# Kernel tuning notes

Hardware: AMD Instinct MI355X
Metric: run time of the kernel (lower is better)

## Reference

```python
import jax, jax.numpy as jnp
import numpy as np

B, T, C, H = 2, 2048, 1024, 16
D = C // H
HID = 4 * C
EPS = 1e-5


def _rmsnorm(x, w):
    return w * (x * jax.lax.rsqrt(jnp.mean(x * x, axis=-1, keepdims=True) + EPS))


def setup_inputs() -> dict:
    key = jax.random.key(0)
    ks = jax.random.split(key, 12)
    s = 0.02
    inp = {
        "x": jax.random.normal(ks[0], (B, T, C), jnp.float32),
        "mask": jnp.tril(jnp.ones((T, T), jnp.int32))[None, None],  # (1,1,T,T) causal
        "attn_norm_w": jnp.ones((C,), jnp.float32),
        "mlp_norm_w": jnp.ones((C,), jnp.float32),
        "q_w": jax.random.normal(ks[1], (C, C), jnp.float32) * s,
        "q_b": jnp.zeros((C,), jnp.float32),
        "k_w": jax.random.normal(ks[2], (C, C), jnp.float32) * s,
        "k_b": jnp.zeros((C,), jnp.float32),
        "v_w": jax.random.normal(ks[3], (C, C), jnp.float32) * s,
        "v_b": jnp.zeros((C,), jnp.float32),
        "o_w": jax.random.normal(ks[4], (C, C), jnp.float32) * s,
        "o_b": jnp.zeros((C,), jnp.float32),
        "w1": jax.random.normal(ks[5], (C, HID), jnp.float32) * s,
        "b1": jnp.zeros((HID,), jnp.float32),
        "w2": jax.random.normal(ks[6], (HID, C), jnp.float32) * s,
        "b2": jnp.zeros((C,), jnp.float32),
    }
    return inp


def reference(x, mask, attn_norm_w, mlp_norm_w, q_w, q_b, k_w, k_b, v_w, v_b,
              o_w, o_b, w1, b1, w2, b2):
    # Pre-norm path (use_post_norm=False)
    h = _rmsnorm(x, attn_norm_w)
    q = (h @ q_w + q_b).reshape(B, T, H, D).transpose(0, 2, 1, 3)  # (B,H,T,D)
    k = (h @ k_w + k_b).reshape(B, T, H, D).transpose(0, 2, 1, 3)
    v = (h @ v_w + v_b).reshape(B, T, H, D).transpose(0, 2, 1, 3)
    scores = jnp.einsum("bhqd,bhkd->bhqk", q, k) / jnp.sqrt(jnp.float32(D))
    scores = jnp.where(mask == 0, jnp.float32(-jnp.inf), scores)
    attn = jax.nn.softmax(scores, axis=-1)  # (B,H,T,T)
    ctx = jnp.einsum("bhqk,bhkd->bhqd", attn, v)
    attn_out = ctx.transpose(0, 2, 1, 3).reshape(B, T, C) @ o_w + o_b
    x = x + attn_out
    m = _rmsnorm(x, mlp_norm_w)
    mlp_out = jax.nn.gelu(m @ w1 + b1, approximate=False) @ w2 + b2
    x = x + mlp_out
    return (x, k, v)
```

## Files before the change

kernel.cpp:

```cpp
#include <hip/hip_runtime.h>
#include <hip/hip_bf16.h>


#define B_ 2
#define T_ 2048
#define C_ 1024
#define H_ 16
#define D_ 64
#define HID_ 4096
#define M_ 4096

typedef __bf16 bf16x8 __attribute__((ext_vector_type(8)));
typedef float f32x4 __attribute__((ext_vector_type(4)));
using bf16 = __hip_bfloat16;

#define WAIT_VM(N) asm volatile("s_waitcnt vmcnt(" #N ")" ::: "memory")
#define SBAR() asm volatile("s_barrier" ::: "memory")

static __device__ __forceinline__ f32x4 mfma16(bf16x8 a, bf16x8 b, f32x4 c) {
  return __builtin_amdgcn_mfma_f32_16x16x32_bf16(a, b, c, 0, 0, 0);
}

static __device__ __forceinline__ void gload16(const bf16* g, bf16* l) {
  __builtin_amdgcn_global_load_lds(
      (const __attribute__((address_space(1))) unsigned int*)g,
      (__attribute__((address_space(3))) unsigned int*)l, 16, 0, 0);
}

static __device__ __forceinline__ unsigned short bfbits(float x) {
  __hip_bfloat16 h = __float2bfloat16(x);
  return *(unsigned short*)&h;
}

static __device__ __forceinline__ float gelu_tanh(float v) {
  float z = 0.7978845608f * (v + 0.044715f * v * v * v);
  float az = fabsf(z);
  float e = __expf(-2.0f * az);
  float th = (1.0f - e) / (1.0f + e);
  th = copysignf(th, z);
  return 0.5f * v * (1.0f + th);
}

__global__ __launch_bounds__(256) void cvt_transpose(const float* __restrict__ in,
                                                     bf16* __restrict__ out, int K, int N) {
  __shared__ float tile[32][33];
  int tid = threadIdx.x, tx = tid & 31, ty = tid >> 5;
  int n0 = blockIdx.x * 32, k0 = blockIdx.y * 32;
#pragma unroll
  for (int i = 0; i < 4; ++i) {
    int r = ty + i * 8;
    tile[r][tx] = in[(size_t)(k0 + r) * N + n0 + tx];
  }
  __syncthreads();
#pragma unroll
  for (int i = 0; i < 4; ++i) {
    int r = ty + i * 8;
    out[(size_t)(n0 + r) * K + k0 + tx] = __float2bfloat16(tile[tx][r]);
  }
}

__global__ __launch_bounds__(256) void pack_bias(const float* __restrict__ q,
                                                 const float* __restrict__ k,
                                                 const float* __restrict__ v,
                                                 float* __restrict__ o) {
  int i = blockIdx.x * 256 + threadIdx.x;
  o[i] = i < 1024 ? q[i] : (i < 2048 ? k[i - 1024] : v[i - 2048]);
}

__global__ __launch_bounds__(256) void rmsnorm_kernel(const float* __restrict__ x,
                                                      const float* __restrict__ w,
                                                      bf16* __restrict__ out) {
  int row = blockIdx.x, tid = threadIdx.x;
  float4 v = ((const float4*)(x + (size_t)row * C_))[tid];
  float ss = v.x * v.x + v.y * v.y + v.z * v.z + v.w * v.w;
#pragma unroll
  for (int d = 1; d < 64; d <<= 1) ss += __shfl_xor(ss, d);
  __shared__ float wsum[4];
  if ((tid & 63) == 0) wsum[tid >> 6] = ss;
  __syncthreads();
  float tot = wsum[0] + wsum[1] + wsum[2] + wsum[3];
  float r = rsqrtf(tot * (1.0f / C_) + 1e-5f);
  float4 wv = ((const float4*)w)[tid];
  bf16* o = out + (size_t)row * C_ + tid * 4;
  o[0] = __float2bfloat16(v.x * wv.x * r);
  o[1] = __float2bfloat16(v.y * wv.y * r);
  o[2] = __float2bfloat16(v.z * wv.z * r);
  o[3] = __float2bfloat16(v.w * wv.w * r);
}

template <int EPI, int DBUF, int SK>
__global__ __launch_bounds__(256) void gemm_kernel(
    const bf16* __restrict__ A, const bf16* __restrict__ Bt, const float* __restrict__ bias,
    bf16* __restrict__ bfout, float* __restrict__ fout, const float* __restrict__ res,
    bf16* __restrict__ vtb, float* __restrict__ paux, const float* __restrict__ bias2,
    int M, int N, int K) {
  __shared__ bf16 Al[(DBUF ? 2 : 1) * 128 * 64];
  __shared__ bf16 Bl[(DBUF ? 2 : 1) * 128 * 64];
  int tid = threadIdx.x, w = tid >> 6, l = tid & 63;
  int g = l >> 4, c = l & 15;
  int nwg = gridDim.x * gridDim.y;
  int bidl = blockIdx.y * gridDim.x + blockIdx.x;
  int wgid = (bidl & 7) * (nwg >> 3) + (bidl >> 3);
  int bx = wgid % gridDim.x, by = wgid / gridDim.x;
  int m0 = by * 128, n0 = bx * 128;
  int wm = (w >> 1) * 64, wn = (w & 1) * 64;
  int Kc = K / SK;
  int kbase = (SK > 1) ? (int)blockIdx.z * Kc : 0;
  int KT = Kc >> 6;
  int lrow = l >> 3;
  int sgr = (l & 7) ^ lrow;

  const bf16* gA = A + (size_t)(m0 + w * 32 + lrow) * K + kbase + sgr * 8;
  const bf16* gB = Bt + (size_t)(n0 + w * 32 + lrow) * K + kbase + sgr * 8;

  auto stage = [&](int kt, int buf) {
#pragma unroll
    for (int i = 0; i < 4; ++i) {
      gload16(gA + (size_t)i * 8 * K + kt * 64, Al + buf * 8192 + (w * 4 + i) * 512);
      gload16(gB + (size_t)i * 8 * K + kt * 64, Bl + buf * 8192 + (w * 4 + i) * 512);
    }
  };
  auto compute = [&](int buf, f32x4 (&acc)[4][4]) {
#pragma unroll
    for (int ch = 0; ch < 2; ++ch) {
      bf16x8 af[4], bfr[4];
#pragma unroll
      for (int f = 0; f < 4; ++f)
        af[f] = *(const bf16x8*)&Al[buf * 8192 + (wm + f * 16 + c) * 64 +
                                    (((ch * 4 + g) ^ (c & 7)) << 3)];
#pragma unroll
      for (int f = 0; f < 4; ++f)
        bfr[f] = *(const bf16x8*)&Bl[buf * 8192 + (wn + f * 16 + c) * 64 +
                                     (((ch * 4 + g) ^ (c & 7)) << 3)];
#pragma unroll
      for (int mf = 0; mf < 4; ++mf)
#pragma unroll
        for (int nf = 0; nf < 4; ++nf) acc[mf][nf] = mfma16(af[mf], bfr[nf], acc[mf][nf]);
    }
  };

  f32x4 acc[4][4] = {};
  if (DBUF) {
    stage(0, 0);
    for (int kt = 0; kt < KT; ++kt) {
      int cur = kt & 1;
      if (kt + 1 < KT) {
        stage(kt + 1, cur ^ 1);
        WAIT_VM(8);
      } else {
        WAIT_VM(0);
      }
      SBAR();
      __builtin_amdgcn_s_setprio(1);
      compute(cur, acc);
      __builtin_amdgcn_s_setprio(0);
      __builtin_amdgcn_sched_barrier(0);
      SBAR();
    }
  } else {
    for (int kt = 0; kt < KT; ++kt) {
      stage(kt, 0);
      __syncthreads();
      compute(0, acc);
      __syncthreads();
    }
  }

#pragma unroll
  for (int mf = 0; mf < 4; ++mf) {
#pragma unroll
    for (int nf = 0; nf < 4; ++nf) {
      int gn = n0 + wn + nf * 16 + c;
      float bv = bias ? bias[gn] : 0.f;
#pragma unroll
      for (int r = 0; r < 4; ++r) {
        int gm = m0 + wm + mf * 16 + g * 4 + r;
        float vr = acc[mf][nf][r];
        float v = vr + bv;
        if (EPI == 4) {
          atomicAdd(fout + (size_t)gm * N + gn, vr);
        } else if (SK > 1 && blockIdx.z > 0) {
          paux[(size_t)gm * N + gn] = vr;
        } else if (EPI == 0) {
          int part = gn >> 10, wi = gn & 1023, hh = wi >> 6, d = wi & 63;
          int b_ = gm >> 11, t = gm & 2047;
          size_t idx = ((size_t)(b_ * H_ + hh) * T_ + t) * D_ + d;
          if (part == 2) {
            vtb[((size_t)(b_ * H_ + hh) * D_ + d) * T_ + t] = __float2bfloat16(v);
            fout[(size_t)2 * 4194304 + idx] = v;
          } else {
            bfout[(size_t)part * 4194304 + idx] = __float2bfloat16(v);
            if (part) fout[(size_t)part * 4194304 + idx] = v;
          }
        } else if (EPI == 3) {
          size_t idx = (size_t)gm * N + gn;
          float t = v + res[idx];
          fout[idx] = t;
          paux[idx] = t + bias2[gn];
        } else {
          size_t idx = (size_t)gm * N + gn;
          bfout[idx] = __float2bfloat16(gelu_tanh(v));
        }
      }
    }
  }
}

__global__ __launch_bounds__(256, 2) void attn_kernel(const bf16* __restrict__ Q,
                                                      const bf16* __restrict__ Kb,
                                                      const bf16* __restrict__ Vt,
                                                      bf16* __restrict__ o0p,
                                                      bf16* __restrict__ o1p,
                                                      float* __restrict__ ml) {
  constexpr int LDP = 72;
  __shared__ bf16 Kl[2][64 * 64];
  __shared__ bf16 Vl[2][64 * 64];
  __shared__ bf16 Pl[4][2][16 * LDP];
  __shared__ float alw[4][2][16];
  int tid = threadIdx.x, w = tid >> 6, l = tid & 63, g = l >> 4, c = l & 15;
  int bid = blockIdx.x;
  int bh = bid & 31;
  int rest = bid >> 5;
  int qt = 15 - (rest >> 1);
  int half = rest & 1;
  int qbase = qt * 128 + w * 32;
  const bf16* Qh = Q + (size_t)bh * T_ * D_;
  const bf16* Kh = Kb + (size_t)bh * T_ * D_;
  const bf16* Vh = Vt + (size_t)bh * T_ * D_;

  int NT = 2 * qt + 2, H0 = qt + 1;
  int t0 = half ? H0 : 0, t1 = half ? NT : H0;

  int srow = l >> 3;
  int sce = ((l & 7) * 8) ^ (srow << 3);
  int cswz = (c & 7) << 3;

  auto stage = [&](int ti, int buf) {
#pragma unroll
    for (int i = 0; i < 2; ++i) {
      int row = i * 32 + w * 8 + srow;
      gload16(&Kh[(size_t)(ti * 64 + row) * D_ + sce], &Kl[buf][i * 2048 + w * 512]);
      gload16(&Vh[(size_t)row * T_ + ti * 64 + sce], &Vl[buf][i * 2048 + w * 512]);
    }
  };

  stage(t0, 0);

  bf16x8 aq[2][2];
#pragma unroll
  for (int qf = 0; qf < 2; ++qf)
#pragma unroll
    for (int ch = 0; ch < 2; ++ch)
      aq[qf][ch] = *(const bf16x8*)&Qh[(size_t)(qbase + qf * 16 + c) * D_ + ch * 32 + g * 8];

  f32x4 o[2][4] = {};
  float mrun[2] = {-1e30f, -1e30f};
  float lrun[2] = {0.f, 0.f};

  __syncthreads();

  for (int ti = t0; ti < t1; ++ti) {
    int cur = (ti - t0) & 1;
    int kv0 = ti * 64;
    if (ti + 1 < t1) stage(ti + 1, cur ^ 1);

    f32x4 sf[2][4];
#pragma unroll
    for (int kb = 0; kb < 4; ++kb) {
      bf16x8 bk0 = *(const bf16x8*)&Kl[cur][(kb * 16 + c) * 64 + ((g * 8) ^ cswz)];
      bf16x8 bk1 = *(const bf16x8*)&Kl[cur][(kb * 16 + c) * 64 + ((32 + g * 8) ^ cswz)];
#pragma unroll
      for (int qf = 0; qf < 2; ++qf) {
        f32x4 t = {};
        t = mfma16(bk0, aq[qf][0], t);
        t = mfma16(bk1, aq[qf][1], t);
        sf[qf][kb] = t;
      }
    }

    float s[2][4][4];
#pragma unroll
    for (int qf = 0; qf < 2; ++qf)
#pragma unroll
      for (int kb = 0; kb < 4; ++kb)
#pragma unroll
        for (int r = 0; r < 4; ++r) s[qf][kb][r] = sf[qf][kb][r] * 0.125f;
    if (kv0 + 63 > qbase) {
#pragma unroll
      for (int qf = 0; qf < 2; ++qf)
#pragma unroll
        for (int kb = 0; kb < 4; ++kb)
#pragma unroll
          for (int r = 0; r < 4; ++r) {
            int qi = qbase + qf * 16 + c;
            int kv = kv0 + kb * 16 + g * 4 + r;
            if (kv > qi) s[qf][kb][r] = -3.0e38f;
          }
    }

#pragma unroll
    for (int qf = 0; qf < 2; ++qf) {
      float m01 = fmaxf(fmaxf(s[qf][0][0], s[qf][0][1]), fmaxf(s[qf][0][2], s[qf][0][3]));
      float m23 = fmaxf(fmaxf(s[qf][1][0], s[qf][1][1]), fmaxf(s[qf][1][2], s[qf][1][3]));
      float m45 = fmaxf(fmaxf(s[qf][2][0], s[qf][2][1]), fmaxf(s[qf][2][2], s[qf][2][3]));
      float m67 = fmaxf(fmaxf(s[qf][3][0], s[qf][3][1]), fmaxf(s[qf][3][2], s[qf][3][3]));
      float tm = fmaxf(fmaxf(m01, m23), fmaxf(m45, m67));
      tm = fmaxf(tm, __shfl_xor(tm, 16));
      tm = fmaxf(tm, __shfl_xor(tm, 32));
      float mn = fmaxf(mrun[qf], tm);
      float al = __expf(mrun[qf] - mn);
      mrun[qf] = mn;
      float asum = 0.f;
#pragma unroll
      for (int kb = 0; kb < 4; ++kb)
#pragma unroll
        for (int r = 0; r < 4; ++r) {
          float pv = __expf(s[qf][kb][r] - mn);
          s[qf][kb][r] = pv;
          asum += pv;
        }
      asum += __shfl_xor(asum, 16);
      asum += __shfl_xor(asum, 32);
      lrun[qf] = lrun[qf] * al + asum;
      if (l < 16) alw[w][qf][c] = al;
    }

#pragma unroll
    for (int qf = 0; qf < 2; ++qf)
#pragma unroll
      for (int kb = 0; kb < 4; ++kb) {
        union { unsigned short u[4]; uint2 v2; } pk;
#pragma unroll
        for (int r = 0; r < 4; ++r) pk.u[r] = bfbits(s[qf][kb][r]);
        *(uint2*)&Pl[w][qf][c * LDP + kb * 16 + g * 4] = pk.v2;
      }

#pragma unroll
    for (int qf = 0; qf < 2; ++qf) {
      f32x4 a4 = *(const f32x4*)&alw[w][qf][g * 4];
#pragma unroll
      for (int db = 0; db < 4; ++db)
#pragma unroll
        for (int r = 0; r < 4; ++r) o[qf][db][r] *= a4[r];
    }

    bf16x8 bvv[4][2];
#pragma unroll
    for (int db = 0; db < 4; ++db)
#pragma unroll
      for (int ck = 0; ck < 2; ++ck)
        bvv[db][ck] = *(const bf16x8*)&Vl[cur][(db * 16 + c) * 64 + ((ck * 32 + g * 8) ^ cswz)];

#pragma unroll
    for (int qf = 0; qf < 2; ++qf) {
      bf16x8 pa0 = *(const bf16x8*)&Pl[w][qf][c * LDP + g * 8];
      bf16x8 pa1 = *(const bf16x8*)&Pl[w][qf][c * LDP + 32 + g * 8];
#pragma unroll
      for (int db = 0; db < 4; ++db) {
        o[qf][db] = mfma16(pa0, bvv[db][0], o[qf][db]);
        o[qf][db] = mfma16(pa1, bvv[db][1], o[qf][db]);
      }
    }
    __syncthreads();
  }

  bf16* op = half ? o1p : o0p;
  int rowbase = bh * 2048 + qbase;
#pragma unroll
  for (int qf = 0; qf < 2; ++qf)
#pragma unroll
    for (int r = 0; r < 4; ++r)
#pragma unroll
      for (int db = 0; db < 4; ++db)
        op[(size_t)(rowbase + qf * 16 + g * 4 + r) * 64 + db * 16 + c] =
            __float2bfloat16(o[qf][db][r]);
  if (l < 16) {
    float* mh = ml + half * 131072;
#pragma unroll
    for (int qf = 0; qf < 2; ++qf) {
      mh[rowbase + qf * 16 + c] = mrun[qf];
      mh[65536 + rowbase + qf * 16 + c] = lrun[qf];
    }
  }
}

__global__ __launch_bounds__(256) void merge_attn(const bf16* __restrict__ o0,
                                                  const bf16* __restrict__ o1,
                                                  const float* __restrict__ ml,
                                                  bf16* __restrict__ ctx) {
  int idx = blockIdx.x * 256 + threadIdx.x;
  int row = idx >> 2, dc = (idx & 3) * 16;
  float m0 = ml[row], l0 = ml[65536 + row];
  float m1 = ml[131072 + row], l1 = ml[196608 + row];
  float Mx = fmaxf(m0, m1);
  float s0 = __expf(m0 - Mx), s1 = __expf(m1 - Mx);
  float inv = 1.0f / (l0 * s0 + l1 * s1);
  const bf16x8* p0 = (const bf16x8*)&o0[(size_t)row * 64 + dc];
  const bf16x8* p1 = (const bf16x8*)&o1[(size_t)row * 64 + dc];
  bf16x8 a0 = p0[0], a1 = p0[1], b0 = p1[0], b1 = p1[1];
  int bh = row >> 11, t = row & 2047;
  int b_ = bh >> 4, hh = bh & 15;
  bf16* dst = ctx + ((size_t)(b_ * T_ + t)) * C_ + hh * D_ + dc;
#pragma unroll
  for (int j = 0; j < 8; ++j) {
    dst[j] = __float2bfloat16(((float)a0[j] * s0 + (float)b0[j] * s1) * inv);
    dst[8 + j] = __float2bfloat16(((float)a1[j] * s0 + (float)b1[j] * s1) * inv);
  }
}

extern "C" void kernel_launch(void* const* d_in, const int* in_sizes, int n_in, void* d_out,
                              int out_size, void* d_ws, size_t ws_size, hipStream_t stream) {
  const float* x = (const float*)d_in[0];
  const float* anw = (const float*)d_in[2];
  const float* mnw = (const float*)d_in[3];
  const float* q_w = (const float*)d_in[4];
  const float* q_b = (const float*)d_in[5];
  const float* k_w = (const float*)d_in[6];
  const float* k_b = (const float*)d_in[7];
  const float* v_w = (const float*)d_in[8];
  const float* v_b = (const float*)d_in[9];
  const float* o_w = (const float*)d_in[10];
  const float* o_b = (const float*)d_in[11];
  const float* w1 = (const float*)d_in[12];
  const float* b1 = (const float*)d_in[13];
  const float* w2 = (const float*)d_in[14];
  const float* b2 = (const float*)d_in[15];
  float* out = (float*)d_out;
  char* ws = (char*)d_ws;

  bf16* qkvT = (bf16*)(ws + 0);
  bf16* owT = (bf16*)(ws + 6291456);
  bf16* w1T = (bf16*)(ws + 8388608);
  bf16* w2T = (bf16*)(ws + 16777216);
  bf16* h = (bf16*)(ws + 25165824);
  bf16* qb = (bf16*)(ws + 33554432);
  bf16* kb = (bf16*)(ws + 41943040);
  bf16* o0p = (bf16*)(ws + 50331648);
  bf16* vtb = (bf16*)(ws + 58720256);
  bf16* ctx = (bf16*)(ws + 67108864);
  bf16* o1p = (bf16*)(ws + 75497472);
  float* ml = (float*)(ws + 25165824);
  float* x2 = (float*)(ws + 33554432);
  bf16* m = h;
  bf16* hid = (bf16*)(ws + 50331648);
  float* qkvb = (float*)(ws + 75497472);

  cvt_transpose<<<dim3(32, 32), 256, 0, stream>>>(q_w, qkvT, 1024, 1024);
  cvt_transpose<<<dim3(32, 32), 256, 0, stream>>>(k_w, qkvT + 1048576, 1024, 1024);
  cvt_transpose<<<dim3(32, 32), 256, 0, stream>>>(v_w, qkvT + 2097152, 1024, 1024);
  cvt_transpose<<<dim3(32, 32), 256, 0, stream>>>(o_w, owT, 1024, 1024);
  cvt_transpose<<<dim3(128, 32), 256, 0, stream>>>(w1, w1T, 1024, 4096);
  cvt_transpose<<<dim3(32, 128), 256, 0, stream>>>(w2, w2T, 4096, 1024);
  pack_bias<<<12, 256, 0, stream>>>(q_b, k_b, v_b, qkvb);

  rmsnorm_kernel<<<4096, 256, 0, stream>>>(x, anw, h);

  gemm_kernel<0, 1, 1><<<dim3(24, 32), 256, 0, stream>>>(
      h, qkvT, qkvb, qb, out, nullptr, vtb, nullptr, nullptr, 4096, 3072, 1024);

  attn_kernel<<<1024, 256, 0, stream>>>(qb, kb, vtb, o0p, o1p, ml);
  merge_attn<<<1024, 256, 0, stream>>>(o0p, o1p, ml, ctx);

  gemm_kernel<3, 1, 1><<<dim3(8, 32), 256, 0, stream>>>(
      ctx, owT, o_b, nullptr, x2, x, nullptr, out, b2, 4096, 1024, 1024);

  rmsnorm_kernel<<<4096, 256, 0, stream>>>(x2, mnw, m);

  gemm_kernel<2, 1, 1><<<dim3(32, 32), 256, 0, stream>>>(
      m, w1T, b1, hid, nullptr, nullptr, nullptr, nullptr, nullptr, 4096, 4096, 1024);
  gemm_kernel<4, 1, 2><<<dim3(8, 32, 2), 256, 0, stream>>>(
      hid, w2T, nullptr, nullptr, out, nullptr, nullptr, nullptr, nullptr, 4096, 1024, 4096);
}
```

Before: 280.0 us.

## Write QKV GEMM output row-major and move head scatter/V transpose to separate kernel

The QKV GEMM epilogue no longer scatters into per-head Q/K layouts, a transposed V and fp32 K/V outputs with strided, uncoalesced stores. It now writes a plain row-major bf16 matrix. A new qkv_post kernel reads the K/V columns, writes the fp32 K/V outputs, and transposes V through shared memory into the layout attention expects. The attention kernel reads Q and K directly from the row-major QKV buffer with stride 3072. This trades the scattered epilogue stores for an extra kernel launch and an extra pass over K/V, and the K output now holds bf16-rounded values instead of fp32 GEMM results.

Result: no change. 275.0 us (-1.8%).

```diff
diff --git a/kernel.cpp b/kernel.cpp
--- a/kernel.cpp
+++ b/kernel.cpp
@@ -9,6 +9,7 @@
 #define D_ 64
 #define HID_ 4096
 #define M_ 4096
+#define NQKV 3072
 
 typedef __bf16 bf16x8 __attribute__((ext_vector_type(8)));
 typedef float f32x4 __attribute__((ext_vector_type(4)));
@@ -88,12 +89,40 @@
   o[3] = __float2bfloat16(v.w * wv.w * r);
 }
 
+__global__ __launch_bounds__(256) void qkv_post(const bf16* __restrict__ Cq,
+                                                bf16* __restrict__ vtb,
+                                                float* __restrict__ kout,
+                                                float* __restrict__ vout) {
+  __shared__ unsigned short vt[64][33];
+  int tid = threadIdx.x, bh = blockIdx.y, t0 = blockIdx.x * 32;
+  int b = bh >> 4, hh = bh & 15;
+  int row = tid >> 3, db8 = (tid & 7) * 8;
+  const bf16* Ck = Cq + (size_t)(b * 2048 + t0) * NQKV + 1024 + hh * 64;
+  bf16x8 kv = *(const bf16x8*)&Ck[(size_t)row * NQKV + db8];
+  float* kd = kout + ((size_t)bh * 2048 + t0 + row) * 64 + db8;
+#pragma unroll
+  for (int j = 0; j < 8; ++j) kd[j] = (float)kv[j];
+  bf16x8 vv = *(const bf16x8*)&Ck[(size_t)row * NQKV + 1024 + db8];
+  const unsigned short* vb = (const unsigned short*)&vv;
+  float* vd = vout + ((size_t)bh * 2048 + t0 + row) * 64 + db8;
+#pragma unroll
+  for (int j = 0; j < 8; ++j) {
+    vd[j] = (float)vv[j];
+    vt[db8 + j][row] = vb[j];
+  }
+  __syncthreads();
+  int d = tid >> 2, t8 = (tid & 3) * 8;
+  union { unsigned short u[8]; bf16x8 v8; } o;
+#pragma unroll
+  for (int j = 0; j < 8; ++j) o.u[j] = vt[d][t8 + j];
+  *(bf16x8*)&vtb[((size_t)bh * 64 + d) * 2048 + t0 + t8] = o.v8;
+}
+
 template <int EPI, int DBUF, int SK>
 __global__ __launch_bounds__(256) void gemm_kernel(
     const bf16* __restrict__ A, const bf16* __restrict__ Bt, const float* __restrict__ bias,
     bf16* __restrict__ bfout, float* __restrict__ fout, const float* __restrict__ res,
-    bf16* __restrict__ vtb, float* __restrict__ paux, const float* __restrict__ bias2,
-    int M, int N, int K) {
+    float* __restrict__ paux, const float* __restrict__ bias2, int M, int N, int K) {
   __shared__ bf16 Al[(DBUF ? 2 : 1) * 128 * 64];
   __shared__ bf16 Bl[(DBUF ? 2 : 1) * 128 * 64];
   int tid = threadIdx.x, w = tid >> 6, l = tid & 63;
@@ -181,17 +210,8 @@
           atomicAdd(fout + (size_t)gm * N + gn, vr);
         } else if (SK > 1 && blockIdx.z > 0) {
           paux[(size_t)gm * N + gn] = vr;
-        } else if (EPI == 0) {
-          int part = gn >> 10, wi = gn & 1023, hh = wi >> 6, d = wi & 63;
-          int b_ = gm >> 11, t = gm & 2047;
-          size_t idx = ((size_t)(b_ * H_ + hh) * T_ + t) * D_ + d;
-          if (part == 2) {
-            vtb[((size_t)(b_ * H_ + hh) * D_ + d) * T_ + t] = __float2bfloat16(v);
-            fout[(size_t)2 * 4194304 + idx] = v;
-          } else {
-            bfout[(size_t)part * 4194304 + idx] = __float2bfloat16(v);
-            if (part) fout[(size_t)part * 4194304 + idx] = v;
-          }
+        } else if (EPI == 5) {
+          bfout[(size_t)gm * N + gn] = __float2bfloat16(v);
         } else if (EPI == 3) {
           size_t idx = (size_t)gm * N + gn;
           float t = v + res[idx];
@@ -206,8 +226,7 @@
   }
 }
 
-__global__ __launch_bounds__(256, 2) void attn_kernel(const bf16* __restrict__ Q,
-                                                      const bf16* __restrict__ Kb,
+__global__ __launch_bounds__(256, 2) void attn_kernel(const bf16* __restrict__ Cq,
                                                       const bf16* __restrict__ Vt,
                                                       bf16* __restrict__ o0p,
                                                       bf16* __restrict__ o1p,
@@ -224,8 +243,9 @@
   int qt = 15 - (rest >> 1);
   int half = rest & 1;
   int qbase = qt * 128 + w * 32;
-  const bf16* Qh = Q + (size_t)bh * T_ * D_;
-  const bf16* Kh = Kb + (size_t)bh * T_ * D_;
+  int b = bh >> 4, hh = bh & 15;
+  const bf16* Qh = Cq + (size_t)(b * 2048) * NQKV + hh * 64;
+  const bf16* Kh = Qh + 1024;
   const bf16* Vh = Vt + (size_t)bh * T_ * D_;
 
   int NT = 2 * qt + 2, H0 = qt + 1;
@@ -239,7 +259,7 @@
 #pragma unroll
     for (int i = 0; i < 2; ++i) {
       int row = i * 32 + w * 8 + srow;
-      gload16(&Kh[(size_t)(ti * 64 + row) * D_ + sce], &Kl[buf][i * 2048 + w * 512]);
+      gload16(&Kh[(size_t)(ti * 64 + row) * NQKV + sce], &Kl[buf][i * 2048 + w * 512]);
       gload16(&Vh[(size_t)row * T_ + ti * 64 + sce], &Vl[buf][i * 2048 + w * 512]);
     }
   };
@@ -251,7 +271,8 @@
   for (int qf = 0; qf < 2; ++qf)
 #pragma unroll
     for (int ch = 0; ch < 2; ++ch)
-      aq[qf][ch] = *(const bf16x8*)&Qh[(size_t)(qbase + qf * 16 + c) * D_ + ch * 32 + g * 8];
+      aq[qf][ch] =
+          *(const bf16x8*)&Qh[(size_t)(qbase + qf * 16 + c) * NQKV + ch * 32 + g * 8];
 
   f32x4 o[2][4] = {};
   float mrun[2] = {-1e30f, -1e30f};
@@ -365,7 +386,7 @@
   }
 
   bf16* op = half ? o1p : o0p;
-  int rowbase = bh * 2048 + qbase;
+  int rowbase = bh * 2048 + qt * 128 + w * 32;
 #pragma unroll
   for (int qf = 0; qf < 2; ++qf)
 #pragma unroll
@@ -428,22 +449,21 @@
   float* out = (float*)d_out;
   char* ws = (char*)d_ws;
 
-  bf16* qkvT = (bf16*)(ws + 0);
-  bf16* owT = (bf16*)(ws + 6291456);
-  bf16* w1T = (bf16*)(ws + 8388608);
-  bf16* w2T = (bf16*)(ws + 16777216);
-  bf16* h = (bf16*)(ws + 25165824);
-  bf16* qb = (bf16*)(ws + 33554432);
-  bf16* kb = (bf16*)(ws + 41943040);
-  bf16* o0p = (bf16*)(ws + 50331648);
+  bf16* owT = (bf16*)(ws + 0);
+  bf16* w1T = (bf16*)(ws + 2097152);
+  bf16* w2T = (bf16*)(ws + 10485760);
+  bf16* h = (bf16*)(ws + 18874368);
+  bf16* qkvT = (bf16*)(ws + 27262976);
+  bf16* Cq = (bf16*)(ws + 33554432);
   bf16* vtb = (bf16*)(ws + 58720256);
-  bf16* ctx = (bf16*)(ws + 67108864);
+  bf16* o0p = (bf16*)(ws + 67108864);
   bf16* o1p = (bf16*)(ws + 75497472);
-  float* ml = (float*)(ws + 25165824);
-  float* x2 = (float*)(ws + 33554432);
+  float* ml = (float*)(ws + 27262976);
+  float* qkvb = (float*)(ws + 67108864);
+  bf16* ctx = (bf16*)(ws + 33554432);
+  float* x2 = (float*)(ws + 41943040);
   bf16* m = h;
   bf16* hid = (bf16*)(ws + 50331648);
-  float* qkvb = (float*)(ws + 75497472);
 
   cvt_transpose<<<dim3(32, 32), 256, 0, stream>>>(q_w, qkvT, 1024, 1024);
   cvt_transpose<<<dim3(32, 32), 256, 0, stream>>>(k_w, qkvT + 1048576, 1024, 1024);
@@ -455,19 +475,21 @@
 
   rmsnorm_kernel<<<4096, 256, 0, stream>>>(x, anw, h);
 
-  gemm_kernel<0, 1, 1><<<dim3(24, 32), 256, 0, stream>>>(
-      h, qkvT, qkvb, qb, out, nullptr, vtb, nullptr, nullptr, 4096, 3072, 1024);
-
-  attn_kernel<<<1024, 256, 0, stream>>>(qb, kb, vtb, o0p, o1p, ml);
+  gemm_kernel<5, 1, 1><<<dim3(24, 32), 256, 0, stream>>>(
+      h, qkvT, qkvb, Cq, nullptr, nullptr, nullptr, nullptr, 4096, 3072, 1024);
+
+  qkv_post<<<dim3(64, 32), 256, 0, stream>>>(Cq, vtb, out + 4194304, out + 8388608);
+
+  attn_kernel<<<1024, 256, 0, stream>>>(Cq, vtb, o0p, o1p, ml);
   merge_attn<<<1024, 256, 0, stream>>>(o0p, o1p, ml, ctx);
 
   gemm_kernel<3, 1, 1><<<dim3(8, 32), 256, 0, stream>>>(
-      ctx, owT, o_b, nullptr, x2, x, nullptr, out, b2, 4096, 1024, 1024);
+      ctx, owT, o_b, nullptr, x2, x, out, b2, 4096, 1024, 1024);
 
   rmsnorm_kernel<<<4096, 256, 0, stream>>>(x2, mnw, m);
 
   gemm_kernel<2, 1, 1><<<dim3(32, 32), 256, 0, stream>>>(
-      m, w1T, b1, hid, nullptr, nullptr, nullptr, nullptr, nullptr, 4096, 4096, 1024);
+      m, w1T, b1, hid, nullptr, nullptr, nullptr, nullptr, 4096, 4096, 1024);
   gemm_kernel<4, 1, 2><<<dim3(8, 32, 2), 256, 0, stream>>>(
-      hid, w2T, nullptr, nullptr, out, nullptr, nullptr, nullptr, nullptr, 4096, 1024, 4096);
-}
+      hid, w2T, nullptr, nullptr, out, nullptr, nullptr, nullptr, 4096, 1024, 4096);
+}
```
